# Optimization experiments

Hardware: AMD Instinct MI355X
Metric: run time of the kernel (lower is better)

Reference implementation:

```python
import jax, jax.numpy as jnp
import numpy as np

V, E, H = 100000, 128, 128  # vocab, embed_dim, lstm_units per direction
B, T = 128, 512             # batch, seq_len


def setup_inputs() -> dict:
    key = jax.random.key(0)
    ks = jax.random.split(key, 16)
    s = 0.05
    x = jax.random.randint(ks[0], (B, T), 0, V)
    emb_table = jax.random.normal(ks[1], (V, E), dtype=jnp.float32) * s
    emb_table = emb_table.at[0].set(0.0)  # padding_idx=0
    def w(k, shape):
        return jax.random.normal(k, shape, dtype=jnp.float32) * s
    return {
        "x": x,
        "emb_table": emb_table,
        "Wih_f": w(ks[2], (4 * H, E)), "Whh_f": w(ks[3], (4 * H, H)),
        "bih_f": w(ks[4], (4 * H,)),  "bhh_f": w(ks[5], (4 * H,)),
        "Wih_b": w(ks[6], (4 * H, E)), "Whh_b": w(ks[7], (4 * H, H)),
        "bih_b": w(ks[8], (4 * H,)),  "bhh_b": w(ks[9], (4 * H,)),
        "W1": w(ks[10], (64, 2 * H)), "b1": w(ks[11], (64,)),
        "W2": w(ks[12], (1, 64)),     "b2": w(ks[13], (1,)),
    }


def _lstm_scan(xp, Whh):
    """xp: (T, B, 4H) precomputed input projection (+biases). Returns hs: (T, B, H)."""
    Hd = Whh.shape[1]

    def step(carry, gx):
        h, c = carry
        g = gx + h @ Whh.T                      # (B, 4H)
        i, f, gg, o = jnp.split(g, 4, axis=-1)  # PyTorch gate order: i, f, g, o
        i = jax.nn.sigmoid(i)
        f = jax.nn.sigmoid(f)
        gg = jnp.tanh(gg)
        o = jax.nn.sigmoid(o)
        c = f * c + i * gg
        h = o * jnp.tanh(c)
        return (h, c), h

    h0 = jnp.zeros((xp.shape[1], Hd), xp.dtype)
    _, hs = jax.lax.scan(step, (h0, h0), xp)
    return hs


def reference(x, emb_table, Wih_f, Whh_f, bih_f, bhh_f,
              Wih_b, Whh_b, bih_b, bhh_b, W1, b1, W2, b2):
    emb = emb_table[x]                                      # (B, T, E)
    # forward direction: precompute input projections for all timesteps
    xp_f = jnp.einsum('bte,ge->tbg', emb, Wih_f) + bih_f + bhh_f  # (T, B, 4H)
    hs_f = _lstm_scan(xp_f, Whh_f)                           # (T, B, H)
    # backward direction: run on time-reversed sequence, then reverse outputs
    xp_b = jnp.einsum('bte,ge->tbg', emb[:, ::-1, :], Wih_b) + bih_b + bhh_b
    hs_b = _lstm_scan(xp_b, Whh_b)[::-1]                     # (T, B, H)
    lstm_out = jnp.concatenate([hs_f, hs_b], axis=-1)        # (T, B, 2H)
    pooled = jnp.max(lstm_out, axis=0)                       # (B, 2H) max over time
    h1 = jax.nn.relu(pooled @ W1.T + b1)                     # dropout = identity (eval)
    return jax.nn.sigmoid(h1 @ W2.T + b2)                    # (B, 1)
```

## Files before the change

kernel.cpp:

```cpp
#include <hip/hip_runtime.h>
#include <hip/hip_fp16.h>

#define TT 512
#define HH 128

typedef _Float16 half2_t __attribute__((ext_vector_type(2)));
typedef _Float16 half4_t __attribute__((ext_vector_type(4)));
typedef _Float16 half8_t __attribute__((ext_vector_type(8)));
typedef float    float4_t __attribute__((ext_vector_type(4)));

__device__ __forceinline__ half2_t h2(float v) {
    half2_t r; r[0] = (_Float16)v; r[1] = (_Float16)v; return r;
}
__device__ __forceinline__ half2_t pkrtz(float a, float b) {
    return __builtin_bit_cast(half2_t, __builtin_amdgcn_cvt_pkrtz(a, b));
}

#define TC1 0.994940f
#define TC3 -0.290799f
#define TC5 0.065507f
#define TC7 -0.0062464f
#define SC1 0.2487350f
#define SC3 -0.0181749f
#define SC5 0.00102355f
#define SC7 -0.0000244141f

__device__ __forceinline__ half2_t tanh_pk(half2_t x) {
    half2_t m = __builtin_elementwise_min(__builtin_elementwise_max(x, h2(-2.0f)), h2(2.0f));
    half2_t t = m * m;
    half2_t p = h2(TC7) * t + h2(TC5);
    p = p * t + h2(TC3);
    p = p * t + h2(TC1);
    return m * p;
}
__device__ __forceinline__ half2_t sigma_pk(half2_t x) {
    half2_t m = __builtin_elementwise_min(__builtin_elementwise_max(x, h2(-4.0f)), h2(4.0f));
    half2_t t = m * m;
    half2_t p = h2(SC7) * t + h2(SC5);
    p = p * t + h2(SC3);
    p = p * t + h2(SC1);
    return m * p + h2(0.5f);
}

__device__ __forceinline__ void wg_barrier_lds() {
#if __has_builtin(__builtin_amdgcn_s_waitcnt)
    __builtin_amdgcn_s_waitcnt(0xC07F);
#else
    asm volatile("s_waitcnt lgkmcnt(0)" ::: "memory");
#endif
    __builtin_amdgcn_s_barrier();
}

__device__ __forceinline__ size_t xp_off(int dirbg, int t, int w, int lane) {
    return (((size_t)dirbg * 512 + t) * 8 + w) * 1024 + (size_t)lane * 16;
}

__global__ __attribute__((amdgpu_flat_work_group_size(512, 512), amdgpu_waves_per_eu(2, 2)))
void xp_gemm_kernel(
    const int* __restrict__ x, const float* __restrict__ emb,
    const float* __restrict__ Wih_f, const float* __restrict__ bih_f, const float* __restrict__ bhh_f,
    const float* __restrict__ Wih_b, const float* __restrict__ bih_b, const float* __restrict__ bhh_b,
    _Float16* __restrict__ xp)
{
    const int wg  = blockIdx.x;
    const int dir = wg >> 3, bg = wg & 7;
    const int tb  = blockIdx.y * 16;

    const float* Wih = dir ? Wih_b : Wih_f;
    const float* bih = dir ? bih_b : bih_f;
    const float* bhh = dir ? bhh_b : bhh_f;

    const int tid = threadIdx.x;
    const int w = tid >> 6, lane = tid & 63, lq = lane >> 4, lm = lane & 15;

    __shared__ int id_sm[256];
    __shared__ _Float16 Esm[256 * 136];

    if (tid < 256)
        id_sm[tid] = x[(size_t)(bg * 16 + (tid >> 4)) * TT + tb + (tid & 15)];

    half8_t awih[4][4];
    #pragma unroll
    for (int T = 0; T < 4; ++T) {
        #pragma unroll
        for (int kk = 0; kk < 4; ++kk) {
            const float4* s = (const float4*)(Wih + (size_t)(T * 128 + w * 16 + lm) * 128 + kk * 32 + lq * 8);
            float4 v0 = s[0], v1 = s[1];
            half8_t h;
            half2_t a = pkrtz(v0.x, v0.y), b = pkrtz(v0.z, v0.w);
            half2_t c = pkrtz(v1.x, v1.y), d = pkrtz(v1.z, v1.w);
            h[0]=a[0]; h[1]=a[1]; h[2]=b[0]; h[3]=b[1];
            h[4]=c[0]; h[5]=c[1]; h[6]=d[0]; h[7]=d[1];
            awih[T][kk] = h;
        }
    }
    float4_t biasv[4];
    #pragma unroll
    for (int T = 0; T < 4; ++T) {
        int g = T * 128 + w * 16 + lq * 4;
        float4 b1 = *(const float4*)(bih + g);
        float4 b2 = *(const float4*)(bhh + g);
        biasv[T] = (float4_t){b1.x + b2.x, b1.y + b2.y, b1.z + b2.z, b1.w + b2.w};
    }
    __syncthreads();

    {
        const int r  = tid >> 1;
        const int hf = tid & 1;
        const int chain = r >> 4, tt2 = r & 15;
        const float* src = emb + (size_t)id_sm[r] * 128 + hf * 64;
        float4 v[16];
        #pragma unroll
        for (int j = 0; j < 16; ++j) v[j] = *(const float4*)(src + 4 * j);
        _Float16* dst = &Esm[(tt2 * 16 + chain) * 136 + hf * 64];
        #pragma unroll
        for (int j = 0; j < 16; ++j) {
            half2_t a = pkrtz(v[j].x, v[j].y), b = pkrtz(v[j].z, v[j].w);
            half4_t q; q[0]=a[0]; q[1]=a[1]; q[2]=b[0]; q[3]=b[1];
            *(half4_t*)(dst + 4 * j) = q;
        }
    }
    __syncthreads();

    #pragma unroll 4
    for (int i = 0; i < 16; ++i) {
        half8_t bfr[4];
        #pragma unroll
        for (int kk = 0; kk < 4; ++kk)
            bfr[kk] = *(const half8_t*)&Esm[(i * 16 + lm) * 136 + kk * 32 + lq * 8];

        float4_t acc[4];
        #pragma unroll
        for (int T = 0; T < 4; ++T) acc[T] = biasv[T];
        #pragma unroll
        for (int kk = 0; kk < 4; ++kk)
            #pragma unroll
            for (int T = 0; T < 4; ++T)
                acc[T] = __builtin_amdgcn_mfma_f32_16x16x32_f16(awih[T][kk], bfr[kk], acc[T], 0, 0, 0);

        half8_t p0, p1;
        {
            half2_t a = pkrtz(acc[0][0], acc[0][1]), b = pkrtz(acc[0][2], acc[0][3]);
            half2_t c = pkrtz(acc[1][0], acc[1][1]), d = pkrtz(acc[1][2], acc[1][3]);
            p0[0]=a[0]; p0[1]=a[1]; p0[2]=b[0]; p0[3]=b[1];
            p0[4]=c[0]; p0[5]=c[1]; p0[6]=d[0]; p0[7]=d[1];
        }
        {
            half2_t a = pkrtz(acc[2][0], acc[2][1]), b = pkrtz(acc[2][2], acc[2][3]);
            half2_t c = pkrtz(acc[3][0], acc[3][1]), d = pkrtz(acc[3][2], acc[3][3]);
            p1[0]=a[0]; p1[1]=a[1]; p1[2]=b[0]; p1[3]=b[1];
            p1[4]=c[0]; p1[5]=c[1]; p1[6]=d[0]; p1[7]=d[1];
        }
        half8_t* dst = (half8_t*)(xp + xp_off(wg, tb + i, w, lane));
        dst[0] = p0; dst[1] = p1;
    }
}

__global__ __attribute__((amdgpu_flat_work_group_size(512, 512), amdgpu_waves_per_eu(2, 2)))
void bilstm_rec_kernel(
    const _Float16* __restrict__ xp,
    const float* __restrict__ Whh_f, const float* __restrict__ Whh_b,
    float* __restrict__ pooled)
{
    const int wg  = blockIdx.x;
    const int dir = wg >> 3, bg = wg & 7;
    const float* Whh = dir ? Whh_b : Whh_f;

    const int tid = threadIdx.x;
    const int w = tid >> 6, lane = tid & 63, lq = lane >> 4, lm = lane & 15;

    __shared__ _Float16 hsm[2][16 * 136];

    half8_t awhh[4][4];
    #pragma unroll
    for (int T = 0; T < 4; ++T) {
        #pragma unroll
        for (int kk = 0; kk < 4; ++kk) {
            const float4* s = (const float4*)(Whh + (size_t)(T * 128 + w * 16 + lm) * 128 + kk * 32 + lq * 8);
            float4 v0 = s[0], v1 = s[1];
            half8_t h;
            half2_t a = pkrtz(v0.x, v0.y), b = pkrtz(v0.z, v0.w);
            half2_t c = pkrtz(v1.x, v1.y), d = pkrtz(v1.z, v1.w);
            h[0]=a[0]; h[1]=a[1]; h[2]=b[0]; h[3]=b[1];
            h[4]=c[0]; h[5]=c[1]; h[6]=d[0]; h[7]=d[1];
            awhh[T][kk] = h;
        }
    }

    for (int k = tid; k < 2 * 16 * 136; k += 512)
        ((_Float16*)hsm)[k] = (_Float16)0.0f;

    const _Float16* xp_wl = xp + ((size_t)wg * 512 * 8 + w) * 1024 + (size_t)lane * 16;

    half8_t Qa[4], Qb[4];
    {
        int ta = dir ? (TT - 1) : 0;
        const half8_t* p = (const half8_t*)(xp_wl + (size_t)ta * 8192);
        Qa[0] = p[0]; Qb[0] = p[1];
    }
    {
        int ta = dir ? (TT - 2) : 1;
        const half8_t* p = (const half8_t*)(xp_wl + (size_t)ta * 8192);
        Qa[1] = p[0]; Qb[1] = p[1];
    }
    __syncthreads();

    const float4_t zz = {0.0f, 0.0f, 0.0f, 0.0f};
    half2_t c01 = h2(0.0f), c23 = h2(0.0f);
    half2_t hm01 = h2(-60000.0f), hm23 = h2(-60000.0f);

    for (int tbs = 0; tbs < TT; tbs += 4) {
        #pragma unroll
        for (int P = 0; P < 4; ++P) {
            const int t = tbs + P;
            {
                int tl = (t + 2 < TT) ? (t + 2) : (TT - 1);
                int ta = dir ? (TT - 1 - tl) : tl;
                const half8_t* pp = (const half8_t*)(xp_wl + (size_t)ta * 8192);
                Qa[(P + 2) & 3] = pp[0]; Qb[(P + 2) & 3] = pp[1];
            }

            half8_t bh[4];
            #pragma unroll
            for (int kk = 0; kk < 4; ++kk)
                bh[kk] = *(const half8_t*)&hsm[P & 1][lm * 136 + kk * 32 + lq * 8];

            float4_t acc[4];
            #pragma unroll
            for (int T = 0; T < 4; ++T)
                acc[T] = __builtin_amdgcn_mfma_f32_16x16x32_f16(awhh[T][0], bh[0], zz, 0, 0, 0);
            #pragma unroll
            for (int kk = 1; kk < 4; ++kk)
                #pragma unroll
                for (int T = 0; T < 4; ++T)
                    acc[T] = __builtin_amdgcn_mfma_f32_16x16x32_f16(awhh[T][kk], bh[kk], acc[T], 0, 0, 0);

            half2_t qa0 = __builtin_shufflevector(Qa[P], Qa[P], 0, 1);
            half2_t qa1 = __builtin_shufflevector(Qa[P], Qa[P], 2, 3);
            half2_t qa2 = __builtin_shufflevector(Qa[P], Qa[P], 4, 5);
            half2_t qa3 = __builtin_shufflevector(Qa[P], Qa[P], 6, 7);
            half2_t qb0 = __builtin_shufflevector(Qb[P], Qb[P], 0, 1);
            half2_t qb1 = __builtin_shufflevector(Qb[P], Qb[P], 2, 3);
            half2_t qb2 = __builtin_shufflevector(Qb[P], Qb[P], 4, 5);
            half2_t qb3 = __builtin_shufflevector(Qb[P], Qb[P], 6, 7);

            half2_t i01 = sigma_pk(pkrtz(acc[0][0], acc[0][1]) + qa0);
            half2_t i23 = sigma_pk(pkrtz(acc[0][2], acc[0][3]) + qa1);
            half2_t f01 = sigma_pk(pkrtz(acc[1][0], acc[1][1]) + qa2);
            half2_t f23 = sigma_pk(pkrtz(acc[1][2], acc[1][3]) + qa3);
            half2_t g01 = tanh_pk(pkrtz(acc[2][0], acc[2][1]) + qb0);
            half2_t g23 = tanh_pk(pkrtz(acc[2][2], acc[2][3]) + qb1);
            half2_t o01 = sigma_pk(pkrtz(acc[3][0], acc[3][1]) + qb2);
            half2_t o23 = sigma_pk(pkrtz(acc[3][2], acc[3][3]) + qb3);

            c01 = f01 * c01 + i01 * g01;
            c23 = f23 * c23 + i23 * g23;
            half2_t h01 = o01 * tanh_pk(c01);
            half2_t h23 = o23 * tanh_pk(c23);
            hm01 = __builtin_elementwise_max(hm01, h01);
            hm23 = __builtin_elementwise_max(hm23, h23);

            half4_t hv4;
            hv4[0] = h01[0]; hv4[1] = h01[1]; hv4[2] = h23[0]; hv4[3] = h23[1];
            *(half4_t*)&hsm[1 - (P & 1)][lm * 136 + w * 16 + lq * 4] = hv4;

            wg_barrier_lds();
        }
    }

    float4 o;
    o.x = (float)hm01[0]; o.y = (float)hm01[1];
    o.z = (float)hm23[0]; o.w = (float)hm23[1];
    *(float4*)&pooled[(size_t)(bg * 16 + lm) * 256 + dir * HH + w * 16 + lq * 4] = o;
}

__global__ __launch_bounds__(64) void mlp_kernel(
    const float* __restrict__ pooled, const float* __restrict__ W1,
    const float* __restrict__ b1, const float* __restrict__ W2,
    const float* __restrict__ b2, float* __restrict__ out)
{
    const int b = blockIdx.x;
    const int j = threadIdx.x;
    const float4* p = (const float4*)(pooled + (size_t)b * 256);
    const float4* wv = (const float4*)(W1 + (size_t)j * 256);
    float s = 0.0f;
    #pragma unroll
    for (int q = 0; q < 64; ++q) {
        float4 pv = p[q];
        float4 ww = wv[q];
        s += pv.x * ww.x + pv.y * ww.y + pv.z * ww.z + pv.w * ww.w;
    }
    s += b1[j];
    s = fmaxf(s, 0.0f);
    float v = W2[j] * s;
    #pragma unroll
    for (int off = 32; off; off >>= 1) v += __shfl_down(v, off);
    if (j == 0) out[b] = 1.0f / (1.0f + __expf(-(v + b2[0])));
}

extern "C" void kernel_launch(void* const* d_in, const int* in_sizes, int n_in,
                              void* d_out, int out_size, void* d_ws, size_t ws_size,
                              hipStream_t stream) {
    const int*   x     = (const int*)d_in[0];
    const float* emb   = (const float*)d_in[1];
    const float* Wih_f = (const float*)d_in[2];
    const float* Whh_f = (const float*)d_in[3];
    const float* bih_f = (const float*)d_in[4];
    const float* bhh_f = (const float*)d_in[5];
    const float* Wih_b = (const float*)d_in[6];
    const float* Whh_b = (const float*)d_in[7];
    const float* bih_b = (const float*)d_in[8];
    const float* bhh_b = (const float*)d_in[9];
    const float* W1    = (const float*)d_in[10];
    const float* b1    = (const float*)d_in[11];
    const float* W2    = (const float*)d_in[12];
    const float* b2    = (const float*)d_in[13];
    float* out = (float*)d_out;

    char* ws = (char*)d_ws;
    float*    pooled = (float*)ws;
    _Float16* xp     = (_Float16*)(ws + 131072);

    hipLaunchKernelGGL(xp_gemm_kernel, dim3(16, 32), dim3(512), 0, stream,
                       x, emb, Wih_f, bih_f, bhh_f, Wih_b, bih_b, bhh_b, xp);
    hipLaunchKernelGGL(bilstm_rec_kernel, dim3(16), dim3(512), 0, stream,
                       xp, Whh_f, Whh_b, pooled);
    hipLaunchKernelGGL(mlp_kernel, dim3(128), dim3(64), 0, stream,
                       pooled, W1, b1, W2, b2, out);
}
```

Baseline: 476.1 us.

## Fuse input projection GEMM into recurrent LSTM kernel with one-step lookahead

Removes the separate input-projection kernel and its fp16 xp buffer in global memory. The recurrent kernel now stages token ids in LDS, gathers the embedding row for step t+2 each step, and computes the next step's input projection with MFMA while the current step runs. The projection result is carried in fp32 as the MFMA accumulator seed instead of being added in fp16. This drops a launch and the global round trip for xp, but adds 16 extra MFMAs and an embedding gather to the serial critical path on only 16 workgroups, plus doubled weight register pressure.

Result: slower. 583.0 us (+22.5%).

```diff
diff --git a/kernel.cpp b/kernel.cpp
--- a/kernel.cpp
+++ b/kernel.cpp
@@ -51,47 +51,50 @@
     __builtin_amdgcn_s_barrier();
 }
 
-__device__ __forceinline__ size_t xp_off(int dirbg, int t, int w, int lane) {
-    return (((size_t)dirbg * 512 + t) * 8 + w) * 1024 + (size_t)lane * 16;
-}
-
 __global__ __attribute__((amdgpu_flat_work_group_size(512, 512), amdgpu_waves_per_eu(2, 2)))
-void xp_gemm_kernel(
+void bilstm_fused_kernel(
     const int* __restrict__ x, const float* __restrict__ emb,
     const float* __restrict__ Wih_f, const float* __restrict__ bih_f, const float* __restrict__ bhh_f,
     const float* __restrict__ Wih_b, const float* __restrict__ bih_b, const float* __restrict__ bhh_b,
-    _Float16* __restrict__ xp)
+    const float* __restrict__ Whh_f, const float* __restrict__ Whh_b,
+    float* __restrict__ pooled)
 {
     const int wg  = blockIdx.x;
     const int dir = wg >> 3, bg = wg & 7;
-    const int tb  = blockIdx.y * 16;
-
     const float* Wih = dir ? Wih_b : Wih_f;
     const float* bih = dir ? bih_b : bih_f;
     const float* bhh = dir ? bhh_b : bhh_f;
+    const float* Whh = dir ? Whh_b : Whh_f;
 
     const int tid = threadIdx.x;
     const int w = tid >> 6, lane = tid & 63, lq = lane >> 4, lm = lane & 15;
-
-    __shared__ int id_sm[256];
-    __shared__ _Float16 Esm[256 * 136];
-
-    if (tid < 256)
-        id_sm[tid] = x[(size_t)(bg * 16 + (tid >> 4)) * TT + tb + (tid & 15)];
-
-    half8_t awih[4][4];
+    const int srow = tid >> 5, sslot = tid & 31;
+
+    __shared__ int x_sm[16 * 512];
+    __shared__ _Float16 esm[2][16 * 136];
+    __shared__ _Float16 hsm[2][16 * 136];
+
+    half8_t awih[4][4], awhh[4][4];
     #pragma unroll
     for (int T = 0; T < 4; ++T) {
         #pragma unroll
         for (int kk = 0; kk < 4; ++kk) {
-            const float4* s = (const float4*)(Wih + (size_t)(T * 128 + w * 16 + lm) * 128 + kk * 32 + lq * 8);
-            float4 v0 = s[0], v1 = s[1];
+            const float4* s1 = (const float4*)(Wih + (size_t)(T * 128 + w * 16 + lm) * 128 + kk * 32 + lq * 8);
+            float4 v0 = s1[0], v1 = s1[1];
             half8_t h;
             half2_t a = pkrtz(v0.x, v0.y), b = pkrtz(v0.z, v0.w);
             half2_t c = pkrtz(v1.x, v1.y), d = pkrtz(v1.z, v1.w);
             h[0]=a[0]; h[1]=a[1]; h[2]=b[0]; h[3]=b[1];
             h[4]=c[0]; h[5]=c[1]; h[6]=d[0]; h[7]=d[1];
             awih[T][kk] = h;
+            const float4* s2 = (const float4*)(Whh + (size_t)(T * 128 + w * 16 + lm) * 128 + kk * 32 + lq * 8);
+            float4 u0 = s2[0], u1 = s2[1];
+            half8_t g;
+            half2_t e = pkrtz(u0.x, u0.y), f = pkrtz(u0.z, u0.w);
+            half2_t gg = pkrtz(u1.x, u1.y), hh = pkrtz(u1.z, u1.w);
+            g[0]=e[0]; g[1]=e[1]; g[2]=f[0]; g[3]=f[1];
+            g[4]=gg[0]; g[5]=gg[1]; g[6]=hh[0]; g[7]=hh[1];
+            awhh[T][kk] = g;
         }
     }
     float4_t biasv[4];
@@ -102,171 +105,115 @@
         float4 b2 = *(const float4*)(bhh + g);
         biasv[T] = (float4_t){b1.x + b2.x, b1.y + b2.y, b1.z + b2.z, b1.w + b2.w};
     }
+
+    for (int k = tid; k < 16 * 512; k += 512)
+        x_sm[k] = x[(size_t)(bg * 16 + (k >> 9)) * TT + (k & 511)];
+    for (int k = tid; k < 2 * 16 * 136; k += 512)
+        ((_Float16*)hsm)[k] = (_Float16)0.0f;
     __syncthreads();
 
     {
-        const int r  = tid >> 1;
-        const int hf = tid & 1;
-        const int chain = r >> 4, tt2 = r & 15;
-        const float* src = emb + (size_t)id_sm[r] * 128 + hf * 64;
-        float4 v[16];
-        #pragma unroll
-        for (int j = 0; j < 16; ++j) v[j] = *(const float4*)(src + 4 * j);
-        _Float16* dst = &Esm[(tt2 * 16 + chain) * 136 + hf * 64];
-        #pragma unroll
-        for (int j = 0; j < 16; ++j) {
-            half2_t a = pkrtz(v[j].x, v[j].y), b = pkrtz(v[j].z, v[j].w);
-            half4_t q; q[0]=a[0]; q[1]=a[1]; q[2]=b[0]; q[3]=b[1];
-            *(half4_t*)(dst + 4 * j) = q;
-        }
+        int t0 = dir ? (TT - 1) : 0;
+        int t1 = dir ? (TT - 2) : 1;
+        int i0 = x_sm[srow * 512 + t0];
+        int i1 = x_sm[srow * 512 + t1];
+        float4 v0 = *(const float4*)(emb + (size_t)i0 * 128 + sslot * 4);
+        float4 v1 = *(const float4*)(emb + (size_t)i1 * 128 + sslot * 4);
+        half2_t a0 = pkrtz(v0.x, v0.y), b0 = pkrtz(v0.z, v0.w);
+        half4_t q0; q0[0]=a0[0]; q0[1]=a0[1]; q0[2]=b0[0]; q0[3]=b0[1];
+        *(half4_t*)&esm[0][srow * 136 + sslot * 4] = q0;
+        half2_t a1 = pkrtz(v1.x, v1.y), b1 = pkrtz(v1.z, v1.w);
+        half4_t q1; q1[0]=a1[0]; q1[1]=a1[1]; q1[2]=b1[0]; q1[3]=b1[1];
+        *(half4_t*)&esm[1][srow * 136 + sslot * 4] = q1;
     }
     __syncthreads();
 
-    #pragma unroll 4
-    for (int i = 0; i < 16; ++i) {
-        half8_t bfr[4];
+    float4_t xpA[4], xpB[4];
+    {
+        half8_t be[4];
         #pragma unroll
         for (int kk = 0; kk < 4; ++kk)
-            bfr[kk] = *(const half8_t*)&Esm[(i * 16 + lm) * 136 + kk * 32 + lq * 8];
-
-        float4_t acc[4];
-        #pragma unroll
-        for (int T = 0; T < 4; ++T) acc[T] = biasv[T];
+            be[kk] = *(const half8_t*)&esm[0][lm * 136 + kk * 32 + lq * 8];
+        #pragma unroll
+        for (int T = 0; T < 4; ++T) xpA[T] = biasv[T];
         #pragma unroll
         for (int kk = 0; kk < 4; ++kk)
             #pragma unroll
             for (int T = 0; T < 4; ++T)
-                acc[T] = __builtin_amdgcn_mfma_f32_16x16x32_f16(awih[T][kk], bfr[kk], acc[T], 0, 0, 0);
-
-        half8_t p0, p1;
-        {
-            half2_t a = pkrtz(acc[0][0], acc[0][1]), b = pkrtz(acc[0][2], acc[0][3]);
-            half2_t c = pkrtz(acc[1][0], acc[1][1]), d = pkrtz(acc[1][2], acc[1][3]);
-            p0[0]=a[0]; p0[1]=a[1]; p0[2]=b[0]; p0[3]=b[1];
-            p0[4]=c[0]; p0[5]=c[1]; p0[6]=d[0]; p0[7]=d[1];
-        }
-        {
-            half2_t a = pkrtz(acc[2][0], acc[2][1]), b = pkrtz(acc[2][2], acc[2][3]);
-            half2_t c = pkrtz(acc[3][0], acc[3][1]), d = pkrtz(acc[3][2], acc[3][3]);
-            p1[0]=a[0]; p1[1]=a[1]; p1[2]=b[0]; p1[3]=b[1];
-            p1[4]=c[0]; p1[5]=c[1]; p1[6]=d[0]; p1[7]=d[1];
-        }
-        half8_t* dst = (half8_t*)(xp + xp_off(wg, tb + i, w, lane));
-        dst[0] = p0; dst[1] = p1;
-    }
-}
-
-__global__ __attribute__((amdgpu_flat_work_group_size(512, 512), amdgpu_waves_per_eu(2, 2)))
-void bilstm_rec_kernel(
-    const _Float16* __restrict__ xp,
-    const float* __restrict__ Whh_f, const float* __restrict__ Whh_b,
-    float* __restrict__ pooled)
-{
-    const int wg  = blockIdx.x;
-    const int dir = wg >> 3, bg = wg & 7;
-    const float* Whh = dir ? Whh_b : Whh_f;
-
-    const int tid = threadIdx.x;
-    const int w = tid >> 6, lane = tid & 63, lq = lane >> 4, lm = lane & 15;
-
-    __shared__ _Float16 hsm[2][16 * 136];
-
-    half8_t awhh[4][4];
-    #pragma unroll
-    for (int T = 0; T < 4; ++T) {
-        #pragma unroll
-        for (int kk = 0; kk < 4; ++kk) {
-            const float4* s = (const float4*)(Whh + (size_t)(T * 128 + w * 16 + lm) * 128 + kk * 32 + lq * 8);
-            float4 v0 = s[0], v1 = s[1];
-            half8_t h;
-            half2_t a = pkrtz(v0.x, v0.y), b = pkrtz(v0.z, v0.w);
-            half2_t c = pkrtz(v1.x, v1.y), d = pkrtz(v1.z, v1.w);
-            h[0]=a[0]; h[1]=a[1]; h[2]=b[0]; h[3]=b[1];
-            h[4]=c[0]; h[5]=c[1]; h[6]=d[0]; h[7]=d[1];
-            awhh[T][kk] = h;
-        }
-    }
-
-    for (int k = tid; k < 2 * 16 * 136; k += 512)
-        ((_Float16*)hsm)[k] = (_Float16)0.0f;
-
-    const _Float16* xp_wl = xp + ((size_t)wg * 512 * 8 + w) * 1024 + (size_t)lane * 16;
-
-    half8_t Qa[4], Qb[4];
-    {
-        int ta = dir ? (TT - 1) : 0;
-        const half8_t* p = (const half8_t*)(xp_wl + (size_t)ta * 8192);
-        Qa[0] = p[0]; Qb[0] = p[1];
-    }
-    {
-        int ta = dir ? (TT - 2) : 1;
-        const half8_t* p = (const half8_t*)(xp_wl + (size_t)ta * 8192);
-        Qa[1] = p[0]; Qb[1] = p[1];
-    }
-    __syncthreads();
-
-    const float4_t zz = {0.0f, 0.0f, 0.0f, 0.0f};
+                xpA[T] = __builtin_amdgcn_mfma_f32_16x16x32_f16(awih[T][kk], be[kk], xpA[T], 0, 0, 0);
+    }
+    wg_barrier_lds();
+
     half2_t c01 = h2(0.0f), c23 = h2(0.0f);
     half2_t hm01 = h2(-60000.0f), hm23 = h2(-60000.0f);
 
-    for (int tbs = 0; tbs < TT; tbs += 4) {
-        #pragma unroll
-        for (int P = 0; P < 4; ++P) {
-            const int t = tbs + P;
-            {
-                int tl = (t + 2 < TT) ? (t + 2) : (TT - 1);
-                int ta = dir ? (TT - 1 - tl) : tl;
-                const half8_t* pp = (const half8_t*)(xp_wl + (size_t)ta * 8192);
-                Qa[(P + 2) & 3] = pp[0]; Qb[(P + 2) & 3] = pp[1];
-            }
-
-            half8_t bh[4];
-            #pragma unroll
-            for (int kk = 0; kk < 4; ++kk)
-                bh[kk] = *(const half8_t*)&hsm[P & 1][lm * 136 + kk * 32 + lq * 8];
-
-            float4_t acc[4];
-            #pragma unroll
-            for (int T = 0; T < 4; ++T)
-                acc[T] = __builtin_amdgcn_mfma_f32_16x16x32_f16(awhh[T][0], bh[0], zz, 0, 0, 0);
-            #pragma unroll
-            for (int kk = 1; kk < 4; ++kk)
-                #pragma unroll
-                for (int T = 0; T < 4; ++T)
-                    acc[T] = __builtin_amdgcn_mfma_f32_16x16x32_f16(awhh[T][kk], bh[kk], acc[T], 0, 0, 0);
-
-            half2_t qa0 = __builtin_shufflevector(Qa[P], Qa[P], 0, 1);
-            half2_t qa1 = __builtin_shufflevector(Qa[P], Qa[P], 2, 3);
-            half2_t qa2 = __builtin_shufflevector(Qa[P], Qa[P], 4, 5);
-            half2_t qa3 = __builtin_shufflevector(Qa[P], Qa[P], 6, 7);
-            half2_t qb0 = __builtin_shufflevector(Qb[P], Qb[P], 0, 1);
-            half2_t qb1 = __builtin_shufflevector(Qb[P], Qb[P], 2, 3);
-            half2_t qb2 = __builtin_shufflevector(Qb[P], Qb[P], 4, 5);
-            half2_t qb3 = __builtin_shufflevector(Qb[P], Qb[P], 6, 7);
-
-            half2_t i01 = sigma_pk(pkrtz(acc[0][0], acc[0][1]) + qa0);
-            half2_t i23 = sigma_pk(pkrtz(acc[0][2], acc[0][3]) + qa1);
-            half2_t f01 = sigma_pk(pkrtz(acc[1][0], acc[1][1]) + qa2);
-            half2_t f23 = sigma_pk(pkrtz(acc[1][2], acc[1][3]) + qa3);
-            half2_t g01 = tanh_pk(pkrtz(acc[2][0], acc[2][1]) + qb0);
-            half2_t g23 = tanh_pk(pkrtz(acc[2][2], acc[2][3]) + qb1);
-            half2_t o01 = sigma_pk(pkrtz(acc[3][0], acc[3][1]) + qb2);
-            half2_t o23 = sigma_pk(pkrtz(acc[3][2], acc[3][3]) + qb3);
-
-            c01 = f01 * c01 + i01 * g01;
-            c23 = f23 * c23 + i23 * g23;
-            half2_t h01 = o01 * tanh_pk(c01);
-            half2_t h23 = o23 * tanh_pk(c23);
-            hm01 = __builtin_elementwise_max(hm01, h01);
-            hm23 = __builtin_elementwise_max(hm23, h23);
-
-            half4_t hv4;
-            hv4[0] = h01[0]; hv4[1] = h01[1]; hv4[2] = h23[0]; hv4[3] = h23[1];
-            *(half4_t*)&hsm[1 - (P & 1)][lm * 136 + w * 16 + lq * 4] = hv4;
-
-            wg_barrier_lds();
-        }
-    }
+    #define FSTEP(T_, XPIN, XPOUT) do {                                             \
+        const int t_ = (T_);                                                        \
+                                          \
+        half8_t bh[4];                                                              \
+        _Pragma("unroll")                                                           \
+        for (int kk = 0; kk < 4; ++kk)                                              \
+            bh[kk] = *(const half8_t*)&hsm[t_ & 1][lm * 136 + kk * 32 + lq * 8];    \
+                       \
+        int k2 = (t_ + 2 < TT) ? (t_ + 2) : (TT - 1);                               \
+        int tau = dir ? (TT - 1 - k2) : k2;                                         \
+        int idxv = x_sm[srow * 512 + tau];                                          \
+        float4 ev = *(const float4*)(emb + (size_t)idxv * 128 + sslot * 4);         \
+                                                               \
+        half8_t be[4];                                                              \
+        _Pragma("unroll")                                                           \
+        for (int kk = 0; kk < 4; ++kk)                                              \
+            be[kk] = *(const half8_t*)&esm[(t_ + 1) & 1][lm * 136 + kk * 32 + lq * 8]; \
+                                                 \
+        float4_t acc[4];                                                            \
+        _Pragma("unroll")                                                           \
+        for (int T = 0; T < 4; ++T)                                                 \
+            acc[T] = __builtin_amdgcn_mfma_f32_16x16x32_f16(awhh[T][0], bh[0], XPIN[T], 0, 0, 0); \
+        _Pragma("unroll")                                                           \
+        for (int kk = 1; kk < 4; ++kk)                                              \
+            _Pragma("unroll")                                                       \
+            for (int T = 0; T < 4; ++T)                                             \
+                acc[T] = __builtin_amdgcn_mfma_f32_16x16x32_f16(awhh[T][kk], bh[kk], acc[T], 0, 0, 0); \
+                      \
+        _Pragma("unroll")                                                           \
+        for (int T = 0; T < 4; ++T)                                                 \
+            XPOUT[T] = __builtin_amdgcn_mfma_f32_16x16x32_f16(awih[T][0], be[0], biasv[T], 0, 0, 0); \
+        _Pragma("unroll")                                                           \
+        for (int kk = 1; kk < 4; ++kk)                                              \
+            _Pragma("unroll")                                                       \
+            for (int T = 0; T < 4; ++T)                                             \
+                XPOUT[T] = __builtin_amdgcn_mfma_f32_16x16x32_f16(awih[T][kk], be[kk], XPOUT[T], 0, 0, 0); \
+                              \
+        half2_t i01 = sigma_pk(pkrtz(acc[0][0], acc[0][1]));                        \
+        half2_t i23 = sigma_pk(pkrtz(acc[0][2], acc[0][3]));                        \
+        half2_t f01 = sigma_pk(pkrtz(acc[1][0], acc[1][1]));                        \
+        half2_t f23 = sigma_pk(pkrtz(acc[1][2], acc[1][3]));                        \
+        half2_t g01 = tanh_pk(pkrtz(acc[2][0], acc[2][1]));                         \
+        half2_t g23 = tanh_pk(pkrtz(acc[2][2], acc[2][3]));                         \
+        half2_t o01 = sigma_pk(pkrtz(acc[3][0], acc[3][1]));                        \
+        half2_t o23 = sigma_pk(pkrtz(acc[3][2], acc[3][3]));                        \
+        c01 = f01 * c01 + i01 * g01;                                                \
+        c23 = f23 * c23 + i23 * g23;                                                \
+        half2_t h01 = o01 * tanh_pk(c01);                                           \
+        half2_t h23 = o23 * tanh_pk(c23);                                           \
+        hm01 = __builtin_elementwise_max(hm01, h01);                                \
+        hm23 = __builtin_elementwise_max(hm23, h23);                                \
+        half4_t hv4;                                                                \
+        hv4[0] = h01[0]; hv4[1] = h01[1]; hv4[2] = h23[0]; hv4[3] = h23[1];         \
+        *(half4_t*)&hsm[1 - (t_ & 1)][lm * 136 + w * 16 + lq * 4] = hv4;            \
+                     \
+        half2_t sa = pkrtz(ev.x, ev.y), sb = pkrtz(ev.z, ev.w);                     \
+        half4_t sq; sq[0]=sa[0]; sq[1]=sa[1]; sq[2]=sb[0]; sq[3]=sb[1];             \
+        *(half4_t*)&esm[t_ & 1][srow * 136 + sslot * 4] = sq;                       \
+        wg_barrier_lds();                                                           \
+    } while (0)
+
+    #pragma unroll 1
+    for (int t = 0; t < TT; t += 2) {
+        FSTEP(t,     xpA, xpB);
+        FSTEP(t + 1, xpB, xpA);
+    }
+    #undef FSTEP
 
     float4 o;
     o.x = (float)hm01[0]; o.y = (float)hm01[1];
@@ -317,14 +264,11 @@
     const float* b2    = (const float*)d_in[13];
     float* out = (float*)d_out;
 
-    char* ws = (char*)d_ws;
-    float*    pooled = (float*)ws;
-    _Float16* xp     = (_Float16*)(ws + 131072);
-
-    hipLaunchKernelGGL(xp_gemm_kernel, dim3(16, 32), dim3(512), 0, stream,
-                       x, emb, Wih_f, bih_f, bhh_f, Wih_b, bih_b, bhh_b, xp);
-    hipLaunchKernelGGL(bilstm_rec_kernel, dim3(16), dim3(512), 0, stream,
-                       xp, Whh_f, Whh_b, pooled);
+    float* pooled = (float*)d_ws;
+
+    hipLaunchKernelGGL(bilstm_fused_kernel, dim3(16), dim3(512), 0, stream,
+                       x, emb, Wih_f, bih_f, bhh_f, Wih_b, bih_b, bhh_b,
+                       Whh_f, Whh_b, pooled);
     hipLaunchKernelGGL(mlp_kernel, dim3(128), dim3(64), 0, stream,
                        pooled, W1, b1, W2, b2, out);
 }
```

## Halve recurrent workgroup to 4 waves, each owning two hidden-unit slices

Applied to the files above, without the earlier changes.

The recurrent LSTM kernel now runs 256 threads (4 waves) per workgroup instead of 512. Each wave holds Whh fragments for two 16-unit hidden slices and issues twice as many MFMAs per step, with the cell and max state doubled. The aim is to make the per-timestep LDS barrier cheaper with fewer waves and to give each wave more independent MFMA work to hide latency. The cost is twice the serial MFMA and activation work per wave on the critical path and higher register pressure, with waves_per_eu set to 1.

Measured after the change: 561.2 us. +17.9%, slower.

```diff
diff --git a/kernel.cpp b/kernel.cpp
--- a/kernel.cpp
+++ b/kernel.cpp
@@ -156,7 +156,7 @@
     }
 }
 
-__global__ __attribute__((amdgpu_flat_work_group_size(512, 512), amdgpu_waves_per_eu(2, 2)))
+__global__ __attribute__((amdgpu_flat_work_group_size(256, 256), amdgpu_waves_per_eu(1, 1)))
 void bilstm_rec_kernel(
     const _Float16* __restrict__ xp,
     const float* __restrict__ Whh_f, const float* __restrict__ Whh_b,
@@ -167,47 +167,56 @@
     const float* Whh = dir ? Whh_b : Whh_f;
 
     const int tid = threadIdx.x;
-    const int w = tid >> 6, lane = tid & 63, lq = lane >> 4, lm = lane & 15;
+    const int wv = tid >> 6;
+    const int lane = tid & 63, lq = lane >> 4, lm = lane & 15;
 
     __shared__ _Float16 hsm[2][16 * 136];
 
-    half8_t awhh[4][4];
-    #pragma unroll
-    for (int T = 0; T < 4; ++T) {
-        #pragma unroll
-        for (int kk = 0; kk < 4; ++kk) {
-            const float4* s = (const float4*)(Whh + (size_t)(T * 128 + w * 16 + lm) * 128 + kk * 32 + lq * 8);
-            float4 v0 = s[0], v1 = s[1];
-            half8_t h;
-            half2_t a = pkrtz(v0.x, v0.y), b = pkrtz(v0.z, v0.w);
-            half2_t c = pkrtz(v1.x, v1.y), d = pkrtz(v1.z, v1.w);
-            h[0]=a[0]; h[1]=a[1]; h[2]=b[0]; h[3]=b[1];
-            h[4]=c[0]; h[5]=c[1]; h[6]=d[0]; h[7]=d[1];
-            awhh[T][kk] = h;
-        }
-    }
-
-    for (int k = tid; k < 2 * 16 * 136; k += 512)
+    half8_t awhh[4][2][4];
+    #pragma unroll
+    for (int T = 0; T < 4; ++T)
+        #pragma unroll
+        for (int p = 0; p < 2; ++p)
+            #pragma unroll
+            for (int kk = 0; kk < 4; ++kk) {
+                const float4* s = (const float4*)(Whh + (size_t)(T * 128 + (2 * wv + p) * 16 + lm) * 128 + kk * 32 + lq * 8);
+                float4 v0 = s[0], v1 = s[1];
+                half8_t h;
+                half2_t a = pkrtz(v0.x, v0.y), b = pkrtz(v0.z, v0.w);
+                half2_t c = pkrtz(v1.x, v1.y), d = pkrtz(v1.z, v1.w);
+                h[0]=a[0]; h[1]=a[1]; h[2]=b[0]; h[3]=b[1];
+                h[4]=c[0]; h[5]=c[1]; h[6]=d[0]; h[7]=d[1];
+                awhh[T][p][kk] = h;
+            }
+
+    for (int k = tid; k < 2 * 16 * 136; k += 256)
         ((_Float16*)hsm)[k] = (_Float16)0.0f;
 
-    const _Float16* xp_wl = xp + ((size_t)wg * 512 * 8 + w) * 1024 + (size_t)lane * 16;
-
-    half8_t Qa[4], Qb[4];
+    const _Float16* xq0 = xp + ((size_t)wg * 512 * 8 + 2 * wv) * 1024 + (size_t)lane * 16;
+    const _Float16* xq1 = xq0 + 1024;
+
+    half8_t Q[4][4];
     {
         int ta = dir ? (TT - 1) : 0;
-        const half8_t* p = (const half8_t*)(xp_wl + (size_t)ta * 8192);
-        Qa[0] = p[0]; Qb[0] = p[1];
+        const half8_t* p0 = (const half8_t*)(xq0 + (size_t)ta * 8192);
+        const half8_t* p1 = (const half8_t*)(xq1 + (size_t)ta * 8192);
+        Q[0][0] = p0[0]; Q[0][1] = p0[1]; Q[0][2] = p1[0]; Q[0][3] = p1[1];
     }
     {
         int ta = dir ? (TT - 2) : 1;
-        const half8_t* p = (const half8_t*)(xp_wl + (size_t)ta * 8192);
-        Qa[1] = p[0]; Qb[1] = p[1];
+        const half8_t* p0 = (const half8_t*)(xq0 + (size_t)ta * 8192);
+        const half8_t* p1 = (const half8_t*)(xq1 + (size_t)ta * 8192);
+        Q[1][0] = p0[0]; Q[1][1] = p0[1]; Q[1][2] = p1[0]; Q[1][3] = p1[1];
     }
     __syncthreads();
 
     const float4_t zz = {0.0f, 0.0f, 0.0f, 0.0f};
-    half2_t c01 = h2(0.0f), c23 = h2(0.0f);
-    half2_t hm01 = h2(-60000.0f), hm23 = h2(-60000.0f);
+    half2_t c01[2], c23[2], hm01[2], hm23[2];
+    #pragma unroll
+    for (int p = 0; p < 2; ++p) {
+        c01[p] = h2(0.0f); c23[p] = h2(0.0f);
+        hm01[p] = h2(-60000.0f); hm23[p] = h2(-60000.0f);
+    }
 
     for (int tbs = 0; tbs < TT; tbs += 4) {
         #pragma unroll
@@ -216,8 +225,10 @@
             {
                 int tl = (t + 2 < TT) ? (t + 2) : (TT - 1);
                 int ta = dir ? (TT - 1 - tl) : tl;
-                const half8_t* pp = (const half8_t*)(xp_wl + (size_t)ta * 8192);
-                Qa[(P + 2) & 3] = pp[0]; Qb[(P + 2) & 3] = pp[1];
+                const half8_t* p0 = (const half8_t*)(xq0 + (size_t)ta * 8192);
+                const half8_t* p1 = (const half8_t*)(xq1 + (size_t)ta * 8192);
+                Q[(P + 2) & 3][0] = p0[0]; Q[(P + 2) & 3][1] = p0[1];
+                Q[(P + 2) & 3][2] = p1[0]; Q[(P + 2) & 3][3] = p1[1];
             }
 
             half8_t bh[4];
@@ -225,53 +236,63 @@
             for (int kk = 0; kk < 4; ++kk)
                 bh[kk] = *(const half8_t*)&hsm[P & 1][lm * 136 + kk * 32 + lq * 8];
 
-            float4_t acc[4];
+            float4_t acc[4][2];
             #pragma unroll
             for (int T = 0; T < 4; ++T)
-                acc[T] = __builtin_amdgcn_mfma_f32_16x16x32_f16(awhh[T][0], bh[0], zz, 0, 0, 0);
+                #pragma unroll
+                for (int p = 0; p < 2; ++p)
+                    acc[T][p] = __builtin_amdgcn_mfma_f32_16x16x32_f16(awhh[T][p][0], bh[0], zz, 0, 0, 0);
             #pragma unroll
             for (int kk = 1; kk < 4; ++kk)
                 #pragma unroll
                 for (int T = 0; T < 4; ++T)
-                    acc[T] = __builtin_amdgcn_mfma_f32_16x16x32_f16(awhh[T][kk], bh[kk], acc[T], 0, 0, 0);
-
-            half2_t qa0 = __builtin_shufflevector(Qa[P], Qa[P], 0, 1);
-            half2_t qa1 = __builtin_shufflevector(Qa[P], Qa[P], 2, 3);
-            half2_t qa2 = __builtin_shufflevector(Qa[P], Qa[P], 4, 5);
-            half2_t qa3 = __builtin_shufflevector(Qa[P], Qa[P], 6, 7);
-            half2_t qb0 = __builtin_shufflevector(Qb[P], Qb[P], 0, 1);
-            half2_t qb1 = __builtin_shufflevector(Qb[P], Qb[P], 2, 3);
-            half2_t qb2 = __builtin_shufflevector(Qb[P], Qb[P], 4, 5);
-            half2_t qb3 = __builtin_shufflevector(Qb[P], Qb[P], 6, 7);
-
-            half2_t i01 = sigma_pk(pkrtz(acc[0][0], acc[0][1]) + qa0);
-            half2_t i23 = sigma_pk(pkrtz(acc[0][2], acc[0][3]) + qa1);
-            half2_t f01 = sigma_pk(pkrtz(acc[1][0], acc[1][1]) + qa2);
-            half2_t f23 = sigma_pk(pkrtz(acc[1][2], acc[1][3]) + qa3);
-            half2_t g01 = tanh_pk(pkrtz(acc[2][0], acc[2][1]) + qb0);
-            half2_t g23 = tanh_pk(pkrtz(acc[2][2], acc[2][3]) + qb1);
-            half2_t o01 = sigma_pk(pkrtz(acc[3][0], acc[3][1]) + qb2);
-            half2_t o23 = sigma_pk(pkrtz(acc[3][2], acc[3][3]) + qb3);
-
-            c01 = f01 * c01 + i01 * g01;
-            c23 = f23 * c23 + i23 * g23;
-            half2_t h01 = o01 * tanh_pk(c01);
-            half2_t h23 = o23 * tanh_pk(c23);
-            hm01 = __builtin_elementwise_max(hm01, h01);
-            hm23 = __builtin_elementwise_max(hm23, h23);
-
-            half4_t hv4;
-            hv4[0] = h01[0]; hv4[1] = h01[1]; hv4[2] = h23[0]; hv4[3] = h23[1];
-            *(half4_t*)&hsm[1 - (P & 1)][lm * 136 + w * 16 + lq * 4] = hv4;
+                    #pragma unroll
+                    for (int p = 0; p < 2; ++p)
+                        acc[T][p] = __builtin_amdgcn_mfma_f32_16x16x32_f16(awhh[T][p][kk], bh[kk], acc[T][p], 0, 0, 0);
+
+            #pragma unroll
+            for (int p = 0; p < 2; ++p) {
+                half2_t qa0 = __builtin_shufflevector(Q[P][2 * p], Q[P][2 * p], 0, 1);
+                half2_t qa1 = __builtin_shufflevector(Q[P][2 * p], Q[P][2 * p], 2, 3);
+                half2_t qa2 = __builtin_shufflevector(Q[P][2 * p], Q[P][2 * p], 4, 5);
+                half2_t qa3 = __builtin_shufflevector(Q[P][2 * p], Q[P][2 * p], 6, 7);
+                half2_t qb0 = __builtin_shufflevector(Q[P][2 * p + 1], Q[P][2 * p + 1], 0, 1);
+                half2_t qb1 = __builtin_shufflevector(Q[P][2 * p + 1], Q[P][2 * p + 1], 2, 3);
+                half2_t qb2 = __builtin_shufflevector(Q[P][2 * p + 1], Q[P][2 * p + 1], 4, 5);
+                half2_t qb3 = __builtin_shufflevector(Q[P][2 * p + 1], Q[P][2 * p + 1], 6, 7);
+
+                half2_t i01 = sigma_pk(pkrtz(acc[0][p][0], acc[0][p][1]) + qa0);
+                half2_t i23 = sigma_pk(pkrtz(acc[0][p][2], acc[0][p][3]) + qa1);
+                half2_t f01 = sigma_pk(pkrtz(acc[1][p][0], acc[1][p][1]) + qa2);
+                half2_t f23 = sigma_pk(pkrtz(acc[1][p][2], acc[1][p][3]) + qa3);
+                half2_t g01 = tanh_pk(pkrtz(acc[2][p][0], acc[2][p][1]) + qb0);
+                half2_t g23 = tanh_pk(pkrtz(acc[2][p][2], acc[2][p][3]) + qb1);
+                half2_t o01 = sigma_pk(pkrtz(acc[3][p][0], acc[3][p][1]) + qb2);
+                half2_t o23 = sigma_pk(pkrtz(acc[3][p][2], acc[3][p][3]) + qb3);
+
+                c01[p] = f01 * c01[p] + i01 * g01;
+                c23[p] = f23 * c23[p] + i23 * g23;
+                half2_t h01 = o01 * tanh_pk(c01[p]);
+                half2_t h23 = o23 * tanh_pk(c23[p]);
+                hm01[p] = __builtin_elementwise_max(hm01[p], h01);
+                hm23[p] = __builtin_elementwise_max(hm23[p], h23);
+
+                half4_t hv4;
+                hv4[0] = h01[0]; hv4[1] = h01[1]; hv4[2] = h23[0]; hv4[3] = h23[1];
+                *(half4_t*)&hsm[1 - (P & 1)][lm * 136 + (2 * wv + p) * 16 + lq * 4] = hv4;
+            }
 
             wg_barrier_lds();
         }
     }
 
-    float4 o;
-    o.x = (float)hm01[0]; o.y = (float)hm01[1];
-    o.z = (float)hm23[0]; o.w = (float)hm23[1];
-    *(float4*)&pooled[(size_t)(bg * 16 + lm) * 256 + dir * HH + w * 16 + lq * 4] = o;
+    #pragma unroll
+    for (int p = 0; p < 2; ++p) {
+        float4 o;
+        o.x = (float)hm01[p][0]; o.y = (float)hm01[p][1];
+        o.z = (float)hm23[p][0]; o.w = (float)hm23[p][1];
+        *(float4*)&pooled[(size_t)(bg * 16 + lm) * 256 + dir * HH + (2 * wv + p) * 16 + lq * 4] = o;
+    }
 }
 
 __global__ __launch_bounds__(64) void mlp_kernel(
@@ -323,7 +344,7 @@
 
     hipLaunchKernelGGL(xp_gemm_kernel, dim3(16, 32), dim3(512), 0, stream,
                        x, emb, Wih_f, bih_f, bhh_f, Wih_b, bih_b, bhh_b, xp);
-    hipLaunchKernelGGL(bilstm_rec_kernel, dim3(16), dim3(512), 0, stream,
+    hipLaunchKernelGGL(bilstm_rec_kernel, dim3(16), dim3(256), 0, stream,
                        xp, Whh_f, Whh_b, pooled);
     hipLaunchKernelGGL(mlp_kernel, dim3(128), dim3(64), 0, stream,
                        pooled, W1, b1, W2, b2, out);
```
